# Kernel tuning notes

Measured on AMD Instinct MI355X. Metric: run time of the kernel, lower is better.

The kernel has to match this reference:

```python
import jax, jax.numpy as jnp
import numpy as np

N_HEADS = 12
D_MODEL = 768
D_HEAD = D_MODEL // N_HEADS
SCALE = D_HEAD ** -0.5
CAUSAL = True


def setup_inputs() -> dict:
    key = jax.random.key(0)
    k0, k1, k2, k3, k4 = jax.random.split(key, 5)
    B, S = 1, 4096
    x = jax.random.normal(k0, (B, S, D_MODEL), dtype=jnp.float32)
    # torch nn.Linear weights: [out_features, in_features]
    W_in = jax.random.normal(k1, (3 * D_MODEL, D_MODEL), dtype=jnp.float32) * (D_MODEL ** -0.5)
    b_in = jax.random.normal(k2, (3 * D_MODEL,), dtype=jnp.float32) * 0.02
    W_out = jax.random.normal(k3, (D_MODEL, D_MODEL), dtype=jnp.float32) * (D_MODEL ** -0.5)
    b_out = jax.random.normal(k4, (D_MODEL,), dtype=jnp.float32) * 0.02
    return {"x": x, "W_in": W_in, "b_in": b_in, "W_out": W_out, "b_out": b_out}


def reference(x, W_in, b_in, W_out, b_out):
    B, S, D = x.shape
    qkv = x @ W_in.T + b_in                      # [B, S, 3D]
    q, k, v = jnp.split(qkv, 3, axis=-1)          # each [B, S, D]
    def heads(t):
        return t.reshape(B, S, N_HEADS, D_HEAD).transpose(0, 2, 1, 3)  # [B, H, S, Dh]
    q, k, v = heads(q), heads(k), heads(v)
    scores = jnp.einsum('bhqd,bhkd->bhqk', q, k) * SCALE  # [B, H, S, S]
    if CAUSAL:
        mask = jnp.tril(jnp.ones((S, S), dtype=bool))
        scores = jnp.where(mask, scores, jnp.float32(-jnp.inf))
    attn = jax.nn.softmax(scores, axis=-1)
    out = jnp.einsum('bhqk,bhkd->bhqd', attn, v)  # [B, H, S, Dh]
    out = out.transpose(0, 2, 1, 3).reshape(B, S, D)
    return out @ W_out.T + b_out
```

## Files before the change

kernel.cpp:

```cpp
#include <hip/hip_runtime.h>
#include <stdint.h>
#include <stddef.h>

#define SEQ    4096
#define DMODEL 768
#define NHEAD  12
#define DHEAD  64
#define QSCALE 0.18033688011112042f
#define M0 28.0f

typedef __attribute__((ext_vector_type(8))) short bf16x8;
typedef __attribute__((ext_vector_type(4))) float f32x4;

__device__ __forceinline__ unsigned short f2bf(float f) {
    union { float f; unsigned int u; } v; v.f = f;
    unsigned int r = v.u + 0x7FFFu + ((v.u >> 16) & 1u);
    return (unsigned short)(r >> 16);
}
__device__ __forceinline__ float bf2f(unsigned short b) {
    union { float f; unsigned int u; } v; v.u = ((unsigned int)b) << 16;
    return v.f;
}
__device__ __forceinline__ unsigned int pktr(float f0, float f1) {
    union { float f; unsigned int u; } a, b; a.f = f0; b.f = f1;
    return (b.u & 0xFFFF0000u) | (a.u >> 16);
}
__device__ __forceinline__ bf16x8 ld8f_bf(const float* p) {
    f32x4 lo = *(const f32x4*)p;
    f32x4 hi = *(const f32x4*)(p + 4);
    union { bf16x8 v; unsigned short u[8]; } pk;
#pragma unroll
    for (int j = 0; j < 4; j++) { pk.u[j] = f2bf(lo[j]); pk.u[4 + j] = f2bf(hi[j]); }
    return pk.v;
}

__global__ __launch_bounds__(256) void cvt_kernel(
    const float* __restrict__ s0, unsigned short* __restrict__ d0, int c0,
    const float* __restrict__ s1, unsigned short* __restrict__ d1, int c1,
    const float* __restrict__ s2, unsigned short* __restrict__ d2)
{
    const int c = blockIdx.x * 256 + threadIdx.x;
    const float* s; unsigned short* d; int base;
    if (c < c0)          { s = s0; d = d0; base = c; }
    else if (c < c0 + c1){ s = s1; d = d1; base = c - c0; }
    else                 { s = s2; d = d2; base = c - c0 - c1; }
    *(bf16x8*)(d + (size_t)base * 8) = ld8f_bf(s + (size_t)base * 8);
}


template <int EPI>
__global__ __launch_bounds__(256, 2) void gemm_bt_kernel(
    const unsigned short* __restrict__ A,
    const unsigned short* __restrict__ B,
    const float* __restrict__ bias,
    int K, int N,
    unsigned short* __restrict__ oq,
    unsigned short* __restrict__ ok,
    unsigned short* __restrict__ ov,
    float* __restrict__ ob)
{
    __shared__ __align__(16) unsigned short As[128 * 72];
    __shared__ __align__(16) unsigned short Bs[128 * 72];

    const int t    = threadIdx.x;
    const int lane = t & 63;
    const int wave = t >> 6;
    const int l15  = lane & 15;
    const int quad = lane >> 4;
    const int wm   = wave >> 1;
    const int wn   = wave & 1;
    const int m0   = blockIdx.y * 128;
    const int n0   = blockIdx.x * 128;

    f32x4 acc[4][4] = {};

    for (int k0 = 0; k0 < K; k0 += 64) {
        bf16x8 ra[4], rb[4];
#pragma unroll
        for (int c = 0; c < 4; c++) {
            int g = c * 256 + t;
            int row = g >> 3, cg = g & 7;
            ra[c] = *(const bf16x8*)(A + (size_t)(m0 + row) * K + (k0 + cg * 8));
            rb[c] = *(const bf16x8*)(B + (size_t)(n0 + row) * K + (k0 + cg * 8));
        }
        __syncthreads();
#pragma unroll
        for (int c = 0; c < 4; c++) {
            int g = c * 256 + t;
            int row = g >> 3, cg = g & 7;
            *(bf16x8*)(As + row * 72 + cg * 8) = ra[c];
            *(bf16x8*)(Bs + row * 72 + cg * 8) = rb[c];
        }
        __syncthreads();
#pragma unroll
        for (int ki = 0; ki < 2; ki++) {
            bf16x8 af[4], bfr[4];
#pragma unroll
            for (int mi = 0; mi < 4; mi++)
                af[mi] = *(const bf16x8*)(As + (wm * 64 + mi * 16 + l15) * 72 + ki * 32 + quad * 8);
#pragma unroll
            for (int ni = 0; ni < 4; ni++)
                bfr[ni] = *(const bf16x8*)(Bs + (wn * 64 + ni * 16 + l15) * 72 + ki * 32 + quad * 8);
#pragma unroll
            for (int mi = 0; mi < 4; mi++)
#pragma unroll
                for (int ni = 0; ni < 4; ni++)
                    acc[mi][ni] = __builtin_amdgcn_mfma_f32_16x16x32_bf16(
                        af[mi], bfr[ni], acc[mi][ni], 0, 0, 0);
        }
    }

    if (EPI == 0) {
        const int nbase = n0 + wn * 64;
        const int which = nbase / DMODEL;
        const int hh    = (nbase % DMODEL) >> 6;
        const size_t hoff = (size_t)hh * SEQ * 64;
        if (which == 0) {
#pragma unroll
            for (int ni = 0; ni < 4; ni++) {
                const int d  = ni * 16 + l15;
                const float bv = bias[nbase + d];
                const int kcq  = d >> 5;
                const int lnq  = ((d & 31) >> 3) * 16;
                const int jq   = d & 7;
#pragma unroll
                for (int mi = 0; mi < 4; mi++) {
                    const int mb = m0 + wm * 64 + mi * 16 + quad * 4;
#pragma unroll
                    for (int r = 0; r < 4; r++) {
                        const int q = mb + r;
                        const size_t off = hoff + (size_t)(q >> 5) * 2048
                            + (((q & 31) >> 4) * 2 + kcq) * 512
                            + (lnq + (q & 15)) * 8 + jq;
                        oq[off] = f2bf((acc[mi][ni][r] + bv) * QSCALE);
                    }
                }
            }
        } else if (which == 1) {
#pragma unroll
            for (int ni = 0; ni < 4; ni++) {
                const int d  = ni * 16 + l15;
                const float bv = bias[nbase + d];
                const int kck  = d >> 5;
                const int lnk  = ((d & 31) >> 3) * 16;
                const int jk   = d & 7;
#pragma unroll
                for (int mi = 0; mi < 4; mi++) {
                    const int mb = m0 + wm * 64 + mi * 16 + quad * 4;
#pragma unroll
                    for (int r = 0; r < 4; r++) {
                        const int s = mb + r;
                        const size_t off = hoff + (size_t)(s >> 6) * 4096
                            + ((((s & 63) >> 4)) * 2 + kck) * 512
                            + (lnk + (s & 15)) * 8 + jk;
                        ok[off] = f2bf(acc[mi][ni][r] + bv);
                    }
                }
            }
        } else {
#pragma unroll
            for (int ni = 0; ni < 4; ni++) {
                const int d  = ni * 16 + l15;
                const float bv = bias[nbase + d];
                const int miv = (d & 63) >> 4;
                const int l15v = d & 15;
#pragma unroll
                for (int mi = 0; mi < 4; mi++) {
                    const int mb = m0 + wm * 64 + mi * 16 + quad * 4;
                    const size_t off = hoff + (size_t)(mb >> 6) * 4096
                        + (miv * 2 + ((mb & 63) >> 5)) * 512
                        + (((mb & 31) >> 3) * 16 + l15v) * 8 + (mb & 7);
                    union { unsigned short u[4]; uint2 v; } pk;
#pragma unroll
                    for (int r = 0; r < 4; r++) pk.u[r] = f2bf(acc[mi][ni][r] + bv);
                    *(uint2*)(ov + off) = pk.v;
                }
            }
        }
    } else {
#pragma unroll
        for (int ni = 0; ni < 4; ni++) {
            const int n  = n0 + wn * 64 + ni * 16 + l15;
            const float bv = bias[n];
#pragma unroll
            for (int mi = 0; mi < 4; mi++) {
                const int mb = m0 + wm * 64 + mi * 16 + quad * 4;
#pragma unroll
                for (int r = 0; r < 4; r++)
                    ob[(size_t)(mb + r) * N + n] = acc[mi][ni][r] + bv;
            }
        }
    }
}

__global__ __launch_bounds__(256) void attn_kernel(
    const unsigned short* __restrict__ Qp,
    const unsigned short* __restrict__ Kp,
    const unsigned short* __restrict__ Vp,
    unsigned short* __restrict__ AO)
{
    __shared__ __align__(16) char LB[21504];

    const int t    = threadIdx.x;
    const int lane = t & 63;
    const int w    = t >> 6;
    const int l15  = lane & 15;
    const int quad = lane >> 4;
    const int h    = blockIdx.y;
    const int px   = blockIdx.x;

    unsigned short* Pw  = (unsigned short*)LB + w * 32 * 72;
    unsigned short* Old = (unsigned short*)LB;
    float*          Lld = (float*)(LB + 20480);

    const unsigned short* Qh = Qp + (size_t)h * SEQ * 64;
    const unsigned short* Kh = Kp + (size_t)h * SEQ * 64;
    const unsigned short* Vh = Vp + (size_t)h * SEQ * 64;

#pragma unroll 1
    for (int phase = 0; phase < 2; phase++) {
        const int qt = (phase == 0 ? (127 - px) : px);
        const int q0 = qt * 32;

        bf16x8 qf[2][2];
#pragma unroll
        for (int qh = 0; qh < 2; qh++)
#pragma unroll
            for (int kc = 0; kc < 2; kc++)
                qf[qh][kc] = *(const bf16x8*)(Qh + (size_t)qt * 2048 + (qh * 2 + kc) * 512 + lane * 8);

        f32x4 o[2][4] = {};
        float lq[2] = { 0.0f, 0.0f };

        const int ntiles = (q0 + 95) >> 6;

        bf16x8 kfn[4][2];
        if (w < ntiles) {
#pragma unroll
            for (int ni = 0; ni < 4; ni++)
#pragma unroll
                for (int kc = 0; kc < 2; kc++)
                    kfn[ni][kc] = *(const bf16x8*)(Kh + (size_t)w * 4096 + (ni * 2 + kc) * 512 + lane * 8);
        }

        for (int tk = w; tk < ntiles; tk += 4) {
            const int k0 = tk * 64;

            f32x4 sc[4][2] = {};
#pragma unroll
            for (int ni = 0; ni < 4; ni++)
#pragma unroll
                for (int qh = 0; qh < 2; qh++)
#pragma unroll
                    for (int kc = 0; kc < 2; kc++)
                        sc[ni][qh] = __builtin_amdgcn_mfma_f32_16x16x32_bf16(
                            kfn[ni][kc], qf[qh][kc], sc[ni][qh], 0, 0, 0);

            bf16x8 vf[4][2];
#pragma unroll
            for (int mi = 0; mi < 4; mi++)
#pragma unroll
                for (int kc = 0; kc < 2; kc++)
                    vf[mi][kc] = *(const bf16x8*)(Vh + (size_t)tk * 4096 + (mi * 2 + kc) * 512 + lane * 8);

            if (tk + 4 < ntiles) {
#pragma unroll
                for (int ni = 0; ni < 4; ni++)
#pragma unroll
                    for (int kc = 0; kc < 2; kc++)
                        kfn[ni][kc] = *(const bf16x8*)(Kh + (size_t)(tk + 4) * 4096 + (ni * 2 + kc) * 512 + lane * 8);
            }

            if (k0 + 63 > q0) {
#pragma unroll
                for (int ni = 0; ni < 4; ni++)
#pragma unroll
                    for (int qh = 0; qh < 2; qh++) {
                        const int q = q0 + qh * 16 + l15;
#pragma unroll
                        for (int r = 0; r < 4; r++) {
                            const int kcol = k0 + ni * 16 + quad * 4 + r;
                            if (kcol > q) sc[ni][qh][r] = -1e30f;
                        }
                    }
            }

#pragma unroll
            for (int ni = 0; ni < 4; ni++)
#pragma unroll
                for (int qh = 0; qh < 2; qh++)
#pragma unroll
                    for (int r = 0; r < 4; r++)
                        sc[ni][qh][r] = exp2f(sc[ni][qh][r] - M0);
#pragma unroll
            for (int qh = 0; qh < 2; qh++)
#pragma unroll
                for (int ni = 0; ni < 4; ni++) {
                    uint2 pv;
                    pv.x = pktr(sc[ni][qh][0], sc[ni][qh][1]);
                    pv.y = pktr(sc[ni][qh][2], sc[ni][qh][3]);
                    *(uint2*)(Pw + (qh * 16 + l15) * 72 + ni * 16 + quad * 4) = pv;
                }

            {
                float b0[4], b1[4];
#pragma unroll
                for (int ni = 0; ni < 4; ni++) {
                    b0[ni] = (sc[ni][0][0] + sc[ni][0][1]) + (sc[ni][0][2] + sc[ni][0][3]);
                    b1[ni] = (sc[ni][1][0] + sc[ni][1][1]) + (sc[ni][1][2] + sc[ni][1][3]);
                }
                lq[0] += (b0[0] + b0[1]) + (b0[2] + b0[3]);
                lq[1] += (b1[0] + b1[1]) + (b1[2] + b1[3]);
            }

            bf16x8 pf[2][2];
#pragma unroll
            for (int qh = 0; qh < 2; qh++)
#pragma unroll
                for (int kc = 0; kc < 2; kc++)
                    pf[qh][kc] = *(const bf16x8*)(Pw + (qh * 16 + l15) * 72 + kc * 32 + quad * 8);

#pragma unroll
            for (int qh = 0; qh < 2; qh++)
#pragma unroll
                for (int mi = 0; mi < 4; mi++)
#pragma unroll
                    for (int kc = 0; kc < 2; kc++)
                        o[qh][mi] = __builtin_amdgcn_mfma_f32_16x16x32_bf16(
                            vf[mi][kc], pf[qh][kc], o[qh][mi], 0, 0, 0);
        }

#pragma unroll
        for (int qh = 0; qh < 2; qh++) {
            lq[qh] += __shfl_xor(lq[qh], 16);
            lq[qh] += __shfl_xor(lq[qh], 32);
        }

        __syncthreads();

#pragma unroll
        for (int qh = 0; qh < 2; qh++)
#pragma unroll
            for (int mi = 0; mi < 4; mi++)
#pragma unroll
                for (int r = 0; r < 4; r++)
                    Old[(w * 64 + mi * 16 + quad * 4 + r) * 40 + qh * 16 + l15] = f2bf(o[qh][mi][r]);
        if (quad == 0) {
#pragma unroll
            for (int qh = 0; qh < 2; qh++)
                Lld[w * 32 + qh * 16 + l15] = lq[qh];
        }
        __syncthreads();

#pragma unroll
        for (int qh = 0; qh < 2; qh++) {
            const int q = qh * 16 + l15;
            const float ltot = (Lld[0 * 32 + q] + Lld[1 * 32 + q])
                             + (Lld[2 * 32 + q] + Lld[3 * 32 + q]);
            const float inv = 1.0f / ltot;
            union { unsigned short u[4]; uint2 v; } pk;
#pragma unroll
            for (int r = 0; r < 4; r++) {
                const int d = w * 16 + quad * 4 + r;
                float a = (bf2f(Old[(0 * 64 + d) * 40 + q]) + bf2f(Old[(1 * 64 + d) * 40 + q]))
                        + (bf2f(Old[(2 * 64 + d) * 40 + q]) + bf2f(Old[(3 * 64 + d) * 40 + q]));
                pk.u[r] = f2bf(a * inv);
            }
            *(uint2*)(AO + (size_t)(q0 + q) * DMODEL + h * DHEAD + w * 16 + quad * 4) = pk.v;
        }
        __syncthreads();
    }
}

extern "C" void kernel_launch(void* const* d_in, const int* in_sizes, int n_in,
                              void* d_out, int out_size, void* d_ws, size_t ws_size,
                              hipStream_t stream)
{
    (void)in_sizes; (void)n_in; (void)out_size; (void)ws_size;

    const float* x     = (const float*)d_in[0];
    const float* W_in  = (const float*)d_in[1];
    const float* b_in  = (const float*)d_in[2];
    const float* W_out = (const float*)d_in[3];
    const float* b_out = (const float*)d_in[4];
    float* out = (float*)d_out;

    char* p = (char*)d_ws;
    const size_t sz_sd = (size_t)SEQ * DMODEL * 2;
    unsigned short* qp   = (unsigned short*)p; p += sz_sd;
    unsigned short* kp   = (unsigned short*)p; p += sz_sd;
    unsigned short* vp   = (unsigned short*)p; p += sz_sd;
    unsigned short* aoxb = (unsigned short*)p; p += sz_sd;
    unsigned short* wb1  = (unsigned short*)p; p += (size_t)3 * DMODEL * DMODEL * 2;
    unsigned short* wb2  = (unsigned short*)p; p += (size_t)DMODEL * DMODEL * 2;

    const int c0 = SEQ * DMODEL / 8;
    const int c1 = 3 * DMODEL * DMODEL / 8;
    const int c2 = DMODEL * DMODEL / 8;

    cvt_kernel<<<(c0 + c1 + c2) / 256, 256, 0, stream>>>(
        x, aoxb, c0, W_in, wb1, c1, W_out, wb2);
    gemm_bt_kernel<0><<<dim3(18, 32), 256, 0, stream>>>(
        aoxb, wb1, b_in, DMODEL, 3 * DMODEL, qp, kp, vp, nullptr);
    attn_kernel<<<dim3(64, 12), 256, 0, stream>>>(qp, kp, vp, aoxb);
    gemm_bt_kernel<1><<<dim3(6, 32), 256, 0, stream>>>(
        aoxb, wb2, b_out, DMODEL, DMODEL, nullptr, nullptr, nullptr, out);
}
```

Measured before the change: 179.4 us.

## Use direct global-to-LDS loads in GEMM, shrink output-projection tile, remap attention blocks

The GEMM tile loads now go straight from global memory into LDS through global_load_lds, with no register staging. This drops the padded LDS stride, so fragment reads may hit more bank conflicts. The GEMM is templated on M tile size, and the output projection uses 64-row tiles to launch twice as many blocks and fill more CUs. The attention kernel also remaps block IDs so that consecutive workgroups spread across heads and query tiles, which changes the XCD/L2 distribution.

```diff
diff --git a/kernel.cpp b/kernel.cpp
--- a/kernel.cpp
+++ b/kernel.cpp
@@ -32,6 +32,12 @@
 #pragma unroll
     for (int j = 0; j < 4; j++) { pk.u[j] = f2bf(lo[j]); pk.u[4 + j] = f2bf(hi[j]); }
     return pk.v;
+}
+__device__ __forceinline__ void gld16(const void* g, void* l) {
+    __builtin_amdgcn_global_load_lds(
+        (const __attribute__((address_space(1))) unsigned int*)g,
+        (__attribute__((address_space(3))) unsigned int*)l,
+        16, 0, 0);
 }
 
 __global__ __launch_bounds__(256) void cvt_kernel(
@@ -48,7 +54,7 @@
 }
 
 
-template <int EPI>
+template <int EPI, int MTILE>
 __global__ __launch_bounds__(256, 2) void gemm_bt_kernel(
     const unsigned short* __restrict__ A,
     const unsigned short* __restrict__ B,
@@ -59,8 +65,11 @@
     unsigned short* __restrict__ ov,
     float* __restrict__ ob)
 {
-    __shared__ __align__(16) unsigned short As[128 * 72];
-    __shared__ __align__(16) unsigned short Bs[128 * 72];
+    constexpr int MICNT = MTILE / 32;
+    constexpr int ACH   = MTILE / 32;
+
+    __shared__ __align__(16) unsigned short As[MTILE * 64];
+    __shared__ __align__(16) unsigned short Bs[128 * 64];
 
     const int t    = threadIdx.x;
     const int lane = t & 63;
@@ -69,40 +78,37 @@
     const int quad = lane >> 4;
     const int wm   = wave >> 1;
     const int wn   = wave & 1;
-    const int m0   = blockIdx.y * 128;
+    const int m0   = blockIdx.y * MTILE;
     const int n0   = blockIdx.x * 128;
 
-    f32x4 acc[4][4] = {};
+    f32x4 acc[MICNT][4] = {};
 
     for (int k0 = 0; k0 < K; k0 += 64) {
-        bf16x8 ra[4], rb[4];
-#pragma unroll
-        for (int c = 0; c < 4; c++) {
-            int g = c * 256 + t;
-            int row = g >> 3, cg = g & 7;
-            ra[c] = *(const bf16x8*)(A + (size_t)(m0 + row) * K + (k0 + cg * 8));
-            rb[c] = *(const bf16x8*)(B + (size_t)(n0 + row) * K + (k0 + cg * 8));
-        }
         __syncthreads();
 #pragma unroll
-        for (int c = 0; c < 4; c++) {
-            int g = c * 256 + t;
-            int row = g >> 3, cg = g & 7;
-            *(bf16x8*)(As + row * 72 + cg * 8) = ra[c];
-            *(bf16x8*)(Bs + row * 72 + cg * 8) = rb[c];
+        for (int j = 0; j < ACH; j++) {
+            const int g = j * 256 + t;
+            gld16(A + (size_t)(m0 + (g >> 3)) * K + (k0 + (g & 7) * 8),
+                  (char*)As + (j * 256 + wave * 64) * 16);
+        }
+#pragma unroll
+        for (int j = 0; j < 4; j++) {
+            const int g = j * 256 + t;
+            gld16(B + (size_t)(n0 + (g >> 3)) * K + (k0 + (g & 7) * 8),
+                  (char*)Bs + (j * 256 + wave * 64) * 16);
         }
         __syncthreads();
 #pragma unroll
         for (int ki = 0; ki < 2; ki++) {
-            bf16x8 af[4], bfr[4];
-#pragma unroll
-            for (int mi = 0; mi < 4; mi++)
-                af[mi] = *(const bf16x8*)(As + (wm * 64 + mi * 16 + l15) * 72 + ki * 32 + quad * 8);
+            bf16x8 af[MICNT], bfr[4];
+#pragma unroll
+            for (int mi = 0; mi < MICNT; mi++)
+                af[mi] = *(const bf16x8*)(As + (wm * (MTILE / 2) + mi * 16 + l15) * 64 + ki * 32 + quad * 8);
 #pragma unroll
             for (int ni = 0; ni < 4; ni++)
-                bfr[ni] = *(const bf16x8*)(Bs + (wn * 64 + ni * 16 + l15) * 72 + ki * 32 + quad * 8);
-#pragma unroll
-            for (int mi = 0; mi < 4; mi++)
+                bfr[ni] = *(const bf16x8*)(Bs + (wn * 64 + ni * 16 + l15) * 64 + ki * 32 + quad * 8);
+#pragma unroll
+            for (int mi = 0; mi < MICNT; mi++)
 #pragma unroll
                 for (int ni = 0; ni < 4; ni++)
                     acc[mi][ni] = __builtin_amdgcn_mfma_f32_16x16x32_bf16(
@@ -124,8 +130,8 @@
                 const int lnq  = ((d & 31) >> 3) * 16;
                 const int jq   = d & 7;
 #pragma unroll
-                for (int mi = 0; mi < 4; mi++) {
-                    const int mb = m0 + wm * 64 + mi * 16 + quad * 4;
+                for (int mi = 0; mi < MICNT; mi++) {
+                    const int mb = m0 + wm * (MTILE / 2) + mi * 16 + quad * 4;
 #pragma unroll
                     for (int r = 0; r < 4; r++) {
                         const int q = mb + r;
@@ -145,8 +151,8 @@
                 const int lnk  = ((d & 31) >> 3) * 16;
                 const int jk   = d & 7;
 #pragma unroll
-                for (int mi = 0; mi < 4; mi++) {
-                    const int mb = m0 + wm * 64 + mi * 16 + quad * 4;
+                for (int mi = 0; mi < MICNT; mi++) {
+                    const int mb = m0 + wm * (MTILE / 2) + mi * 16 + quad * 4;
 #pragma unroll
                     for (int r = 0; r < 4; r++) {
                         const int s = mb + r;
@@ -165,8 +171,8 @@
                 const int miv = (d & 63) >> 4;
                 const int l15v = d & 15;
 #pragma unroll
-                for (int mi = 0; mi < 4; mi++) {
-                    const int mb = m0 + wm * 64 + mi * 16 + quad * 4;
+                for (int mi = 0; mi < MICNT; mi++) {
+                    const int mb = m0 + wm * (MTILE / 2) + mi * 16 + quad * 4;
                     const size_t off = hoff + (size_t)(mb >> 6) * 4096
                         + (miv * 2 + ((mb & 63) >> 5)) * 512
                         + (((mb & 31) >> 3) * 16 + l15v) * 8 + (mb & 7);
@@ -183,8 +189,8 @@
             const int n  = n0 + wn * 64 + ni * 16 + l15;
             const float bv = bias[n];
 #pragma unroll
-            for (int mi = 0; mi < 4; mi++) {
-                const int mb = m0 + wm * 64 + mi * 16 + quad * 4;
+            for (int mi = 0; mi < MICNT; mi++) {
+                const int mb = m0 + wm * (MTILE / 2) + mi * 16 + quad * 4;
 #pragma unroll
                 for (int r = 0; r < 4; r++)
                     ob[(size_t)(mb + r) * N + n] = acc[mi][ni][r] + bv;
@@ -206,8 +212,11 @@
     const int w    = t >> 6;
     const int l15  = lane & 15;
     const int quad = lane >> 4;
-    const int h    = blockIdx.y;
-    const int px   = blockIdx.x;
+
+    const int id   = blockIdx.y * 64 + blockIdx.x;
+    const int v    = (id & 7) * 96 + (id >> 3);
+    const int h    = v >> 6;
+    const int px   = v & 63;
 
     unsigned short* Pw  = (unsigned short*)LB + w * 32 * 72;
     unsigned short* Old = (unsigned short*)LB;
@@ -400,9 +409,9 @@
 
     cvt_kernel<<<(c0 + c1 + c2) / 256, 256, 0, stream>>>(
         x, aoxb, c0, W_in, wb1, c1, W_out, wb2);
-    gemm_bt_kernel<0><<<dim3(18, 32), 256, 0, stream>>>(
+    gemm_bt_kernel<0, 128><<<dim3(18, 32), 256, 0, stream>>>(
         aoxb, wb1, b_in, DMODEL, 3 * DMODEL, qp, kp, vp, nullptr);
     attn_kernel<<<dim3(64, 12), 256, 0, stream>>>(qp, kp, vp, aoxb);
-    gemm_bt_kernel<1><<<dim3(6, 32), 256, 0, stream>>>(
+    gemm_bt_kernel<1, 64><<<dim3(6, 64), 256, 0, stream>>>(
         aoxb, wb2, b_out, DMODEL, DMODEL, nullptr, nullptr, nullptr, out);
 }
```

After: 178.6 us. No clear change (-0.5%).
